# Kernel tuning notes

Hardware: AMD Instinct MI355X
Metric: run time of the kernel (lower is better)

## Reference

```python
import jax, jax.numpy as jnp
import numpy as np

CELL = 50.0  # cubic box edge length (self.cell)
N_ATOMS = 100000
N_PAIRS = 6400000
N_TABLE = 1024
EPS = 1e-12


def setup_inputs() -> dict:
    key = jax.random.key(0)
    k1, k2, k3 = jax.random.split(key, 3)
    # positions inside the box
    q = jax.random.uniform(k1, (N_ATOMS, 3), dtype=jnp.float32) * CELL
    # neighbor pair list [E,2] (each pair listed once; forces scattered to both ends)
    nbr_list = jax.random.randint(k2, (N_PAIRS, 2), 0, N_ATOMS, dtype=jnp.int32)
    # tabulated force: r grid (sorted, covers max minimum-image distance) and force values
    r_max = CELL * np.sqrt(3.0) / 2.0
    table_r = jnp.linspace(0.1, r_max, N_TABLE, dtype=jnp.float32)
    table_f = jax.random.normal(k3, (N_TABLE,), dtype=jnp.float32)
    return {"q": q, "nbr_list": nbr_list, "table_r": table_r, "table_f": table_f}


def reference(q, nbr_list, table_r, table_f):
    i = nbr_list[:, 0]
    j = nbr_list[:, 1]
    # pair displacement with minimum-image convention in a cubic cell
    d = q[i] - q[j]                                  # [E,3]
    d = d - CELL * jnp.round(d / CELL)
    pdist = jnp.sqrt(jnp.sum(d * d, axis=-1, keepdims=True))  # [E,1]
    unit_vector = d / jnp.maximum(pdist, EPS)        # [E,3]
    # tabulated force magnitude lookup (GPU-side interpolation replacing scipy interp1d)
    force_magnitude = jnp.interp(pdist[:, 0], table_r, table_f)[:, None]  # [E,1]
    force_vector = force_magnitude * unit_vector     # [E,3]
    # scatter-add to atoms (index_add_ on dim 0, + on i, - on j)
    force = jnp.zeros_like(q).at[i].add(force_vector).at[j].add(-force_vector)
    return force
```

## Files before the change

### kernel.cpp

```cpp
#include <hip/hip_runtime.h>

#define CELL 50.0f
#define N_TABLE 1024
#define NB 1024
#define NBLK 512
#define THREADS 256
#define SCAT_THREADS 512
#define LBUF_CAP 25088
#define RED_THREADS 512
#define NREP 8
#define BATCH 6

typedef unsigned int uint;
typedef unsigned long long ull;

__global__ __launch_bounds__(THREADS) void pack_q4_kernel(
    const float* __restrict__ q, float4* __restrict__ q4, int n_atoms)
{
    int i = blockIdx.x * THREADS + threadIdx.x;
    if (i < n_atoms)
        q4[i] = make_float4(q[3 * i], q[3 * i + 1], q[3 * i + 2], 0.0f);
}

__global__ __launch_bounds__(THREADS) void hist_kernel(
    const int2* __restrict__ nbr, uint* __restrict__ partial,
    uint* __restrict__ rawh, int n_pairs, int ppb)
{
    __shared__ uint h[NB];
    for (int k = threadIdx.x; k < NB; k += THREADS) h[k] = 0;
    __syncthreads();
    int start = blockIdx.x * ppb;
    int end   = min(start + ppb, n_pairs & ~1);
    const int4* nbr4 = (const int4*)nbr;
    for (int p2 = (start >> 1) + threadIdx.x; p2 < (end >> 1); p2 += THREADS) {
        int4 v = nbr4[p2];
        atomicAdd(&h[((uint)v.x) >> 7], 1u);
        atomicAdd(&h[((uint)v.y) >> 7], 1u);
        atomicAdd(&h[((uint)v.z) >> 7], 1u);
        atomicAdd(&h[((uint)v.w) >> 7], 1u);
    }
    if (blockIdx.x == 0 && threadIdx.x == 0 && (n_pairs & 1)) {
        int2 ij = nbr[n_pairs - 1];
        atomicAdd(&h[((uint)ij.x) >> 7], 1u);
        atomicAdd(&h[((uint)ij.y) >> 7], 1u);
    }
    __syncthreads();
    for (int k = threadIdx.x; k < NB; k += THREADS) {
        uint c = h[k];
        partial[k * NBLK + blockIdx.x] = c;
        rawh[blockIdx.x * NB + k]      = c;
    }
}

__global__ __launch_bounds__(THREADS) void scan_rows_kernel(
    uint* __restrict__ partial, uint* __restrict__ binTotal)
{
    __shared__ uint s[THREADS];
    int bin = blockIdx.x;
    uint running = 0;
    for (int c = 0; c < NBLK / THREADS; c++) {
        int idx = bin * NBLK + c * THREADS + threadIdx.x;
        uint v = partial[idx];
        s[threadIdx.x] = v;
        __syncthreads();
        for (int off = 1; off < THREADS; off <<= 1) {
            uint t = (threadIdx.x >= (uint)off) ? s[threadIdx.x - off] : 0u;
            __syncthreads();
            s[threadIdx.x] += t;
            __syncthreads();
        }
        partial[idx] = running + s[threadIdx.x] - v;
        uint csum = s[THREADS - 1];
        __syncthreads();
        running += csum;
    }
    if (threadIdx.x == 0) binTotal[bin] = running;
}

__global__ __launch_bounds__(THREADS) void scan_totals_kernel(
    const uint* __restrict__ binTotal, uint* __restrict__ binBase)
{
    __shared__ uint s[THREADS];
    uint v[4];
    uint sum = 0;
    int base = threadIdx.x * 4;
    for (int k = 0; k < 4; k++) { v[k] = binTotal[base + k]; sum += v[k]; }
    s[threadIdx.x] = sum;
    __syncthreads();
    for (int off = 1; off < THREADS; off <<= 1) {
        uint t = (threadIdx.x >= (uint)off) ? s[threadIdx.x - off] : 0u;
        __syncthreads();
        s[threadIdx.x] += t;
        __syncthreads();
    }
    uint run = s[threadIdx.x] - sum;
    for (int k = 0; k < 4; k++) { binBase[base + k] = run; run += v[k]; }
    if (threadIdx.x == THREADS - 1) binBase[NB] = run;
}

__global__ __launch_bounds__(SCAT_THREADS) void scatter_sorted_kernel(
    const int2* __restrict__ nbr, const uint* __restrict__ rawh,
    const uint* __restrict__ partial, const uint* __restrict__ binBase,
    uint* __restrict__ entries, int n_pairs, int ppb)
{
    __shared__ uint lbuf[LBUF_CAP];
    __shared__ uint localBase[NB];
    __shared__ uint lcur[NB];
    __shared__ uint gcur[NB];
    __shared__ uint ssc[SCAT_THREADS];

    int tid = threadIdx.x;
    int blk = blockIdx.x;

    for (int k = tid; k < NB; k += SCAT_THREADS)
        gcur[k] = binBase[k] + partial[k * NBLK + blk];

    uint v0 = rawh[blk * NB + 2 * tid];
    uint v1 = rawh[blk * NB + 2 * tid + 1];
    uint sum2 = v0 + v1;
    ssc[tid] = sum2;
    __syncthreads();
    for (int off = 1; off < SCAT_THREADS; off <<= 1) {
        uint t = (tid >= off) ? ssc[tid - off] : 0u;
        __syncthreads();
        ssc[tid] += t;
        __syncthreads();
    }
    uint base = ssc[tid] - sum2;
    localBase[2 * tid]     = base;      lcur[2 * tid]     = base;
    localBase[2 * tid + 1] = base + v0; lcur[2 * tid + 1] = base + v0;
    __syncthreads();

    int start = blk * ppb;
    int end   = min(start + ppb, n_pairs & ~1);
    const int4* nbr4 = (const int4*)nbr;
    int lim = end >> 1;
    int p2  = (start >> 1) + tid;
    if (p2 < lim) {
        int4 v = nbr4[p2];
        for (;;) {
            int pn = p2 + SCAT_THREADS;
            int4 vnext;
            bool has = pn < lim;
            if (has) vnext = nbr4[pn];
            uint i0 = (uint)v.x, j0 = (uint)v.y, i1 = (uint)v.z, j1 = (uint)v.w;
            uint o0 = atomicAdd(&lcur[i0 >> 7], 1u);
            uint o1 = atomicAdd(&lcur[j0 >> 7], 1u);
            uint o2 = atomicAdd(&lcur[i1 >> 7], 1u);
            uint o3 = atomicAdd(&lcur[j1 >> 7], 1u);
            lbuf[o0] = (j0 << 7) | (i0 & 127u);
            lbuf[o1] = (i0 << 7) | (j0 & 127u);
            lbuf[o2] = (j1 << 7) | (i1 & 127u);
            lbuf[o3] = (i1 << 7) | (j1 & 127u);
            if (!has) break;
            v = vnext; p2 = pn;
        }
    }
    if (blk == 0 && tid == 0 && (n_pairs & 1)) {
        int2 ij = nbr[n_pairs - 1];
        uint i = (uint)ij.x, j = (uint)ij.y;
        uint o;
        o = atomicAdd(&lcur[i >> 7], 1u); lbuf[o] = (j << 7) | (i & 127u);
        o = atomicAdd(&lcur[j >> 7], 1u); lbuf[o] = (i << 7) | (j & 127u);
    }
    __syncthreads();

    int wave = tid >> 6, lane = tid & 63;
    for (int b = wave; b < NB; b += SCAT_THREADS / 64) {
        uint lb  = localBase[b];
        uint cnt = lcur[b] - lb;
        if (!cnt) continue;
        uint gdst = gcur[b];
        for (uint o = lane; o < cnt; o += 64)
            entries[gdst + o] = lbuf[lb + o];
    }
}

__global__ __launch_bounds__(THREADS) void scatter_plain_kernel(
    const int2* __restrict__ nbr, const uint* __restrict__ partial,
    const uint* __restrict__ binBase, uint* __restrict__ entries,
    int n_pairs, int ppb)
{
    __shared__ uint cur[NB];
    for (int k = threadIdx.x; k < NB; k += THREADS)
        cur[k] = binBase[k] + partial[k * NBLK + blockIdx.x];
    __syncthreads();
    int start = blockIdx.x * ppb;
    int end   = min(start + ppb, n_pairs & ~1);
    const int4* nbr4 = (const int4*)nbr;
    for (int p2 = (start >> 1) + threadIdx.x; p2 < (end >> 1); p2 += THREADS) {
        int4 v = nbr4[p2];
        uint i0 = (uint)v.x, j0 = (uint)v.y, i1 = (uint)v.z, j1 = (uint)v.w;
        uint p;
        p = atomicAdd(&cur[i0 >> 7], 1u); entries[p] = (j0 << 7) | (i0 & 127u);
        p = atomicAdd(&cur[j0 >> 7], 1u); entries[p] = (i0 << 7) | (j0 & 127u);
        p = atomicAdd(&cur[i1 >> 7], 1u); entries[p] = (j1 << 7) | (i1 & 127u);
        p = atomicAdd(&cur[j1 >> 7], 1u); entries[p] = (i1 << 7) | (j1 & 127u);
    }
    if (blockIdx.x == 0 && threadIdx.x == 0 && (n_pairs & 1)) {
        int2 ij = nbr[n_pairs - 1];
        uint i = (uint)ij.x, j = (uint)ij.y;
        uint p;
        p = atomicAdd(&cur[i >> 7], 1u); entries[p] = (j << 7) | (i & 127u);
        p = atomicAdd(&cur[j >> 7], 1u); entries[p] = (i << 7) | (j & 127u);
    }
}

__device__ __forceinline__ void proc_entry(
    uint ev, float ox, float oy, float oz,
    const float4* __restrict__ qs, const float2* __restrict__ tfp,
    float4* __restrict__ accw, float r0, float inv_dr, int lane)
{
    int local = (int)(ev & 127u);
    float4 m = qs[local];
    float dx = m.x - ox, dy = m.y - oy, dz = m.z - oz;
    dx -= (dx > 25.0f) ? 50.0f : ((dx < -25.0f) ? -50.0f : 0.0f);
    dy -= (dy > 25.0f) ? 50.0f : ((dy < -25.0f) ? -50.0f : 0.0f);
    dz -= (dz > 25.0f) ? 50.0f : ((dz < -25.0f) ? -50.0f : 0.0f);
    float r2 = dx * dx + dy * dy + dz * dz;
    float rs = __builtin_amdgcn_rsqf(fmaxf(r2, 1e-24f));
    float r  = r2 * rs;
    float t  = (r - r0) * inv_dr;
    t = fminf(fmaxf(t, 0.0f), 1023.0f);
    int idx = min((int)t, N_TABLE - 2);
    float frac = t - (float)idx;
    float2 tp = tfp[idx];
    float s = (tp.x + frac * tp.y) * rs;
    float fx = s * dx, fy = s * dy, fz = s * dz;

    ull m64 = __ballot(1);
    #pragma unroll
    for (int b = 0; b < 7; b++) {
        ull bb = __ballot((local >> b) & 1);
        m64 &= ((local >> b) & 1) ? bb : ~bb;
    }
    ull self = 1ull << lane;
    bool leader = ((m64 & (self - 1ull)) == 0ull);
    ull rem = leader ? (m64 & ~self) : 0ull;

    while (__any(rem != 0ull)) {
        int src = rem ? (int)__builtin_ctzll(rem) : lane;
        float px = __shfl(fx, src);
        float py = __shfl(fy, src);
        float pz = __shfl(fz, src);
        if (rem) {
            fx += px; fy += py; fz += pz;
            rem &= rem - 1ull;
        }
    }
    if (leader) {
        float4 a = accw[local];
        a.x += fx; a.y += fy; a.z += fz;
        accw[local] = a;
    }
}

template<int USE_Q4>
__global__ __launch_bounds__(RED_THREADS, 8) void reduce_kernel(
    const float* __restrict__ q, const float4* __restrict__ q4,
    const float* __restrict__ table_r, const float* __restrict__ table_f,
    const uint* __restrict__ binBase, const uint* __restrict__ entries,
    float* __restrict__ force, int n_atoms)
{
    __shared__ float2 tfp[N_TABLE];
    __shared__ float4 qs[128];
    __shared__ float4 accv[NREP * 128];

    int b = blockIdx.x;
    int atomBase = b << 7;
    if (atomBase >= n_atoms) return;
    int nA = min(128, n_atoms - atomBase);
    int lane = threadIdx.x & 63;

    const float r0     = table_r[0];
    const float rend   = table_r[N_TABLE - 1];
    const float inv_dr = (float)(N_TABLE - 1) / (rend - r0);

    for (int k = threadIdx.x; k < N_TABLE - 1; k += RED_THREADS) {
        float a = table_f[k], c = table_f[k + 1];
        tfp[k] = make_float2(a, c - a);
    }
    for (int k = threadIdx.x; k < nA; k += RED_THREADS) {
        if (USE_Q4) qs[k] = q4[atomBase + k];
        else qs[k] = make_float4(q[(atomBase + k) * 3], q[(atomBase + k) * 3 + 1],
                                 q[(atomBase + k) * 3 + 2], 0.0f);
    }
    for (int k = threadIdx.x; k < NREP * 128; k += RED_THREADS)
        accv[k] = make_float4(0.0f, 0.0f, 0.0f, 0.0f);
    __syncthreads();

    float4* accw = &accv[(threadIdx.x >> 6) * 128];

    uint e0 = binBase[b], e1 = binBase[b + 1];
    uint count = e1 - e0;
    const uint CHUNK = BATCH * RED_THREADS;
    uint nmain = (count / CHUNK) * CHUNK;

    if (nmain) {
        uint v[BATCH];
        #pragma unroll
        for (int k = 0; k < BATCH; k++)
            v[k] = entries[e0 + threadIdx.x + k * RED_THREADS];

        for (uint base = 0; base < nmain; ) {
            float ox[BATCH], oy[BATCH], oz[BATCH];
            #pragma unroll
            for (int k = 0; k < BATCH; k++) {
                uint other = v[k] >> 7;
                if (USE_Q4) {
                    const float* p = (const float*)&q4[other];
                    ox[k] = p[0]; oy[k] = p[1]; oz[k] = p[2];
                } else {
                    ox[k] = q[3 * other]; oy[k] = q[3 * other + 1]; oz[k] = q[3 * other + 2];
                }
            }
            uint base_n = base + CHUNK;
            uint vn[BATCH];
            if (base_n < nmain) {
                #pragma unroll
                for (int k = 0; k < BATCH; k++)
                    vn[k] = entries[e0 + base_n + threadIdx.x + k * RED_THREADS];
            } else {
                #pragma unroll
                for (int k = 0; k < BATCH; k++) vn[k] = 0u;
            }
            #pragma unroll
            for (int k = 0; k < BATCH; k++)
                proc_entry(v[k], ox[k], oy[k], oz[k], qs, tfp, accw, r0, inv_dr, lane);
            #pragma unroll
            for (int k = 0; k < BATCH; k++) v[k] = vn[k];
            base = base_n;
        }
    }
    for (uint e = e0 + nmain + threadIdx.x; e < e1; e += RED_THREADS) {
        uint ev = entries[e];
        uint other = ev >> 7;
        float ox, oy, oz;
        if (USE_Q4) {
            const float* p = (const float*)&q4[other];
            ox = p[0]; oy = p[1]; oz = p[2];
        } else {
            ox = q[3 * other]; oy = q[3 * other + 1]; oz = q[3 * other + 2];
        }
        proc_entry(ev, ox, oy, oz, qs, tfp, accw, r0, inv_dr, lane);
    }

    __syncthreads();
    for (int k = threadIdx.x; k < nA; k += RED_THREADS) {
        float sx = 0.0f, sy = 0.0f, sz = 0.0f;
        #pragma unroll
        for (int rp = 0; rp < NREP; rp++) {
            float4 a = accv[rp * 128 + k];
            sx += a.x; sy += a.y; sz += a.z;
        }
        force[(atomBase + k) * 3 + 0] = sx;
        force[(atomBase + k) * 3 + 1] = sy;
        force[(atomBase + k) * 3 + 2] = sz;
    }
}

__global__ __launch_bounds__(THREADS) void pair_force_atomic_kernel(
    const float* __restrict__ q, const int2* __restrict__ nbr,
    const float* __restrict__ table_r, const float* __restrict__ table_f,
    float* __restrict__ force, int n_pairs)
{
    __shared__ float tr[N_TABLE];
    __shared__ float tf[N_TABLE];
    for (int k = threadIdx.x; k < N_TABLE; k += THREADS) { tr[k] = table_r[k]; tf[k] = table_f[k]; }
    __syncthreads();
    const float r0 = tr[0], rend = tr[N_TABLE - 1];
    const float inv_dr = (float)(N_TABLE - 1) / (rend - r0);
    int p = blockIdx.x * THREADS + threadIdx.x;
    if (p >= n_pairs) return;
    int2 ij = nbr[p];
    int i = ij.x, j = ij.y;
    float dx = q[3 * i] - q[3 * j], dy = q[3 * i + 1] - q[3 * j + 1], dz = q[3 * i + 2] - q[3 * j + 2];
    dx -= CELL * rintf(dx / CELL); dy -= CELL * rintf(dy / CELL); dz -= CELL * rintf(dz / CELL);
    float r = sqrtf(dx * dx + dy * dy + dz * dz);
    float inv = 1.0f / fmaxf(r, 1e-12f);
    float fm;
    if (r <= r0) fm = tf[0];
    else if (r >= rend) fm = tf[N_TABLE - 1];
    else {
        float t = (r - r0) * inv_dr;
        int idx = min(max((int)t, 0), N_TABLE - 2);
        if (r < tr[idx]) idx = max(idx - 1, 0);
        else if (r >= tr[idx + 1]) idx = min(idx + 1, N_TABLE - 2);
        float rl = tr[idx], rh = tr[idx + 1];
        fm = tf[idx] + (r - rl) * (tf[idx + 1] - tf[idx]) / (rh - rl);
    }
    float s = fm * inv;
    float fx = s * dx, fy = s * dy, fz = s * dz;
    atomicAdd(&force[3 * i + 0], fx); atomicAdd(&force[3 * i + 1], fy); atomicAdd(&force[3 * i + 2], fz);
    atomicAdd(&force[3 * j + 0], -fx); atomicAdd(&force[3 * j + 1], -fy); atomicAdd(&force[3 * j + 2], -fz);
}

extern "C" void kernel_launch(void* const* d_in, const int* in_sizes, int n_in,
                              void* d_out, int out_size, void* d_ws, size_t ws_size,
                              hipStream_t stream) {
    const float* q       = (const float*)d_in[0];
    const int2*  nbr     = (const int2*)d_in[1];
    const float* table_r = (const float*)d_in[2];
    const float* table_f = (const float*)d_in[3];
    float*       force   = (float*)d_out;

    const int n_pairs = in_sizes[1] / 2;
    const int n_atoms = in_sizes[0] / 3;

    size_t off_partial  = 0;
    size_t off_rawh     = (off_partial + (size_t)NB * NBLK * 4 + 255) & ~255ull;
    size_t off_binTotal = (off_rawh + (size_t)NB * NBLK * 4 + 255) & ~255ull;
    size_t off_binBase  = (off_binTotal + (size_t)NB * 4 + 255) & ~255ull;
    size_t off_entries  = (off_binBase + (size_t)(NB + 1) * 4 + 255) & ~255ull;
    size_t off_q4       = (off_entries + (size_t)2 * n_pairs * 4 + 255) & ~255ull;
    size_t need_base    = off_q4;
    size_t need_q4      = off_q4 + (size_t)n_atoms * 16;

    if (ws_size < need_base || n_atoms > NB * 128) {
        hipMemsetAsync(d_out, 0, (size_t)out_size * sizeof(float), stream);
        int blocks = (n_pairs + THREADS - 1) / THREADS;
        pair_force_atomic_kernel<<<blocks, THREADS, 0, stream>>>(q, nbr, table_r, table_f, force, n_pairs);
        return;
    }

    char* ws = (char*)d_ws;
    uint*   partial  = (uint*)(ws + off_partial);
    uint*   rawh     = (uint*)(ws + off_rawh);
    uint*   binTotal = (uint*)(ws + off_binTotal);
    uint*   binBase  = (uint*)(ws + off_binBase);
    uint*   entries  = (uint*)(ws + off_entries);
    float4* q4       = (float4*)(ws + off_q4);
    int use_q4 = (ws_size >= need_q4) ? 1 : 0;

    int ppb = (((n_pairs + NBLK - 1) / NBLK) + 1) & ~1;

    if (use_q4) {
        int pb = (n_atoms + THREADS - 1) / THREADS;
        pack_q4_kernel<<<pb, THREADS, 0, stream>>>(q, q4, n_atoms);
    }
    hist_kernel<<<NBLK, THREADS, 0, stream>>>(nbr, partial, rawh, n_pairs, ppb);
    scan_rows_kernel<<<NB, THREADS, 0, stream>>>(partial, binTotal);
    scan_totals_kernel<<<1, THREADS, 0, stream>>>(binTotal, binBase);
    if (2 * ppb <= LBUF_CAP)
        scatter_sorted_kernel<<<NBLK, SCAT_THREADS, 0, stream>>>(
            nbr, rawh, partial, binBase, entries, n_pairs, ppb);
    else
        scatter_plain_kernel<<<NBLK, THREADS, 0, stream>>>(
            nbr, partial, binBase, entries, n_pairs, ppb);
    if (use_q4)
        reduce_kernel<1><<<NB, RED_THREADS, 0, stream>>>(q, q4, table_r, table_f, binBase, entries, force, n_atoms);
    else
        reduce_kernel<0><<<NB, RED_THREADS, 0, stream>>>(q, q4, table_r, table_f, binBase, entries, force, n_atoms);
}
```

Before: 171.2 us.

## Sort bin entries by local atom in shared memory and accumulate in registers

The reduce kernel now counting-sorts each bin's entries by local atom index in shared memory, in phases of up to 9216 entries. Four threads then share each atom and accumulate its forces in registers. This replaces the per-entry ballot/shuffle wave-level match-and-reduce and the replicated shared-memory accumulators. The cost is an extra histogram, scan and scatter pass with several block barriers per phase, load imbalance when atoms have uneven neighbour counts, and larger shared memory use that may lower occupancy.

```diff
diff --git a/kernel.cpp b/kernel.cpp
--- a/kernel.cpp
+++ b/kernel.cpp
@@ -8,8 +8,7 @@
 #define SCAT_THREADS 512
 #define LBUF_CAP 25088
 #define RED_THREADS 512
-#define NREP 8
-#define BATCH 6
+#define PHASE_CAP 9216
 
 typedef unsigned int uint;
 typedef unsigned long long ull;
@@ -206,14 +205,12 @@
     }
 }
 
-__device__ __forceinline__ void proc_entry(
-    uint ev, float ox, float oy, float oz,
-    const float4* __restrict__ qs, const float2* __restrict__ tfp,
-    float4* __restrict__ accw, float r0, float inv_dr, int lane)
-{
-    int local = (int)(ev & 127u);
-    float4 m = qs[local];
-    float dx = m.x - ox, dy = m.y - oy, dz = m.z - oz;
+__device__ __forceinline__ void phys_acc(
+    float ax, float ay, float az, float ox, float oy, float oz,
+    const float* __restrict__ tfa, const float* __restrict__ tfd,
+    float r0, float inv_dr, float& fx, float& fy, float& fz)
+{
+    float dx = ax - ox, dy = ay - oy, dz = az - oz;
     dx -= (dx > 25.0f) ? 50.0f : ((dx < -25.0f) ? -50.0f : 0.0f);
     dy -= (dy > 25.0f) ? 50.0f : ((dy < -25.0f) ? -50.0f : 0.0f);
     dz -= (dz > 25.0f) ? 50.0f : ((dz < -25.0f) ? -50.0f : 0.0f);
@@ -224,135 +221,129 @@
     t = fminf(fmaxf(t, 0.0f), 1023.0f);
     int idx = min((int)t, N_TABLE - 2);
     float frac = t - (float)idx;
-    float2 tp = tfp[idx];
-    float s = (tp.x + frac * tp.y) * rs;
-    float fx = s * dx, fy = s * dy, fz = s * dz;
-
-    ull m64 = __ballot(1);
-    #pragma unroll
-    for (int b = 0; b < 7; b++) {
-        ull bb = __ballot((local >> b) & 1);
-        m64 &= ((local >> b) & 1) ? bb : ~bb;
-    }
-    ull self = 1ull << lane;
-    bool leader = ((m64 & (self - 1ull)) == 0ull);
-    ull rem = leader ? (m64 & ~self) : 0ull;
-
-    while (__any(rem != 0ull)) {
-        int src = rem ? (int)__builtin_ctzll(rem) : lane;
-        float px = __shfl(fx, src);
-        float py = __shfl(fy, src);
-        float pz = __shfl(fz, src);
-        if (rem) {
-            fx += px; fy += py; fz += pz;
-            rem &= rem - 1ull;
-        }
-    }
-    if (leader) {
-        float4 a = accw[local];
-        a.x += fx; a.y += fy; a.z += fz;
-        accw[local] = a;
-    }
+    float sm = (tfa[idx] + frac * tfd[idx]) * rs;
+    fx += sm * dx; fy += sm * dy; fz += sm * dz;
 }
 
 template<int USE_Q4>
-__global__ __launch_bounds__(RED_THREADS, 8) void reduce_kernel(
+__global__ __launch_bounds__(RED_THREADS) void reduce_sorted_kernel(
     const float* __restrict__ q, const float4* __restrict__ q4,
     const float* __restrict__ table_r, const float* __restrict__ table_f,
     const uint* __restrict__ binBase, const uint* __restrict__ entries,
     float* __restrict__ force, int n_atoms)
 {
-    __shared__ float2 tfp[N_TABLE];
-    __shared__ float4 qs[128];
-    __shared__ float4 accv[NREP * 128];
-
-    int b = blockIdx.x;
+    __shared__ float tfa[N_TABLE];
+    __shared__ float tfd[N_TABLE];
+    __shared__ uint  sorted[PHASE_CAP];
+    __shared__ uint  hcnt[128], hcur[128], hstart[128], sscan[128];
+    __shared__ float paccx[RED_THREADS], paccy[RED_THREADS], paccz[RED_THREADS];
+
+    int b = blockIdx.x, tid = threadIdx.x;
     int atomBase = b << 7;
     if (atomBase >= n_atoms) return;
     int nA = min(128, n_atoms - atomBase);
-    int lane = threadIdx.x & 63;
 
     const float r0     = table_r[0];
     const float rend   = table_r[N_TABLE - 1];
     const float inv_dr = (float)(N_TABLE - 1) / (rend - r0);
 
-    for (int k = threadIdx.x; k < N_TABLE - 1; k += RED_THREADS) {
-        float a = table_f[k], c = table_f[k + 1];
-        tfp[k] = make_float2(a, c - a);
-    }
-    for (int k = threadIdx.x; k < nA; k += RED_THREADS) {
-        if (USE_Q4) qs[k] = q4[atomBase + k];
-        else qs[k] = make_float4(q[(atomBase + k) * 3], q[(atomBase + k) * 3 + 1],
-                                 q[(atomBase + k) * 3 + 2], 0.0f);
-    }
-    for (int k = threadIdx.x; k < NREP * 128; k += RED_THREADS)
-        accv[k] = make_float4(0.0f, 0.0f, 0.0f, 0.0f);
-    __syncthreads();
-
-    float4* accw = &accv[(threadIdx.x >> 6) * 128];
+    for (int k = tid; k < N_TABLE - 1; k += RED_THREADS) {
+        float a = table_f[k];
+        tfa[k] = a; tfd[k] = table_f[k + 1] - a;
+    }
+    paccx[tid] = 0.0f; paccy[tid] = 0.0f; paccz[tid] = 0.0f;
+
+    int a = tid & 127, s4 = tid >> 7;
+    float ax = 0.0f, ay = 0.0f, az = 0.0f;
+    if (a < nA) {
+        if (USE_Q4) { float4 v = q4[atomBase + a]; ax = v.x; ay = v.y; az = v.z; }
+        else {
+            ax = q[(atomBase + a) * 3];
+            ay = q[(atomBase + a) * 3 + 1];
+            az = q[(atomBase + a) * 3 + 2];
+        }
+    }
 
     uint e0 = binBase[b], e1 = binBase[b + 1];
-    uint count = e1 - e0;
-    const uint CHUNK = BATCH * RED_THREADS;
-    uint nmain = (count / CHUNK) * CHUNK;
-
-    if (nmain) {
-        uint v[BATCH];
-        #pragma unroll
-        for (int k = 0; k < BATCH; k++)
-            v[k] = entries[e0 + threadIdx.x + k * RED_THREADS];
-
-        for (uint base = 0; base < nmain; ) {
-            float ox[BATCH], oy[BATCH], oz[BATCH];
-            #pragma unroll
-            for (int k = 0; k < BATCH; k++) {
-                uint other = v[k] >> 7;
+
+    for (uint es = e0; es < e1; es += PHASE_CAP) {
+        uint ee = min(es + PHASE_CAP, e1);
+
+        if (tid < 128) hcnt[tid] = 0;
+        __syncthreads();
+
+        for (uint e = es + tid; e < ee; e += RED_THREADS)
+            atomicAdd(&hcnt[entries[e] & 127u], 1u);
+        __syncthreads();
+
+        if (tid < 128) sscan[tid] = hcnt[tid];
+        __syncthreads();
+        for (int off = 1; off < 128; off <<= 1) {
+            uint t = 0;
+            if (tid < 128 && tid >= off) t = sscan[tid - off];
+            __syncthreads();
+            if (tid < 128) sscan[tid] += t;
+            __syncthreads();
+        }
+        if (tid < 128) {
+            uint s0 = sscan[tid] - hcnt[tid];
+            hstart[tid] = s0; hcur[tid] = s0;
+        }
+        __syncthreads();
+
+        for (uint e = es + tid; e < ee; e += RED_THREADS) {
+            uint ev = entries[e];
+            uint p  = atomicAdd(&hcur[ev & 127u], 1u);
+            sorted[p] = ev >> 7;
+        }
+        __syncthreads();
+
+        {
+            uint st  = hstart[a];
+            uint cnt = hcnt[a];
+            uint chunk = (cnt + 3) >> 2;
+            uint k0 = min((uint)s4 * chunk, cnt);
+            uint k1 = min(k0 + chunk, cnt);
+            float fx = 0.0f, fy = 0.0f, fz = 0.0f;
+
+            uint k = k0;
+            for (; k + 4 <= k1; k += 4) {
+                uint o0 = sorted[st + k],     o1 = sorted[st + k + 1];
+                uint o2 = sorted[st + k + 2], o3 = sorted[st + k + 3];
+                float x0, y0, z0, x1, y1, z1, x2, y2, z2, x3, y3, z3;
                 if (USE_Q4) {
-                    const float* p = (const float*)&q4[other];
-                    ox[k] = p[0]; oy[k] = p[1]; oz[k] = p[2];
+                    float4 g0 = q4[o0], g1 = q4[o1], g2 = q4[o2], g3 = q4[o3];
+                    x0 = g0.x; y0 = g0.y; z0 = g0.z;
+                    x1 = g1.x; y1 = g1.y; z1 = g1.z;
+                    x2 = g2.x; y2 = g2.y; z2 = g2.z;
+                    x3 = g3.x; y3 = g3.y; z3 = g3.z;
                 } else {
-                    ox[k] = q[3 * other]; oy[k] = q[3 * other + 1]; oz[k] = q[3 * other + 2];
+                    x0 = q[3*o0]; y0 = q[3*o0+1]; z0 = q[3*o0+2];
+                    x1 = q[3*o1]; y1 = q[3*o1+1]; z1 = q[3*o1+2];
+                    x2 = q[3*o2]; y2 = q[3*o2+1]; z2 = q[3*o2+2];
+                    x3 = q[3*o3]; y3 = q[3*o3+1]; z3 = q[3*o3+2];
                 }
+                phys_acc(ax, ay, az, x0, y0, z0, tfa, tfd, r0, inv_dr, fx, fy, fz);
+                phys_acc(ax, ay, az, x1, y1, z1, tfa, tfd, r0, inv_dr, fx, fy, fz);
+                phys_acc(ax, ay, az, x2, y2, z2, tfa, tfd, r0, inv_dr, fx, fy, fz);
+                phys_acc(ax, ay, az, x3, y3, z3, tfa, tfd, r0, inv_dr, fx, fy, fz);
             }
-            uint base_n = base + CHUNK;
-            uint vn[BATCH];
-            if (base_n < nmain) {
-                #pragma unroll
-                for (int k = 0; k < BATCH; k++)
-                    vn[k] = entries[e0 + base_n + threadIdx.x + k * RED_THREADS];
-            } else {
-                #pragma unroll
-                for (int k = 0; k < BATCH; k++) vn[k] = 0u;
+            for (; k < k1; ++k) {
+                uint o = sorted[st + k];
+                float ox, oy, oz;
+                if (USE_Q4) { float4 g = q4[o]; ox = g.x; oy = g.y; oz = g.z; }
+                else { ox = q[3*o]; oy = q[3*o+1]; oz = q[3*o+2]; }
+                phys_acc(ax, ay, az, ox, oy, oz, tfa, tfd, r0, inv_dr, fx, fy, fz);
             }
-            #pragma unroll
-            for (int k = 0; k < BATCH; k++)
-                proc_entry(v[k], ox[k], oy[k], oz[k], qs, tfp, accw, r0, inv_dr, lane);
-            #pragma unroll
-            for (int k = 0; k < BATCH; k++) v[k] = vn[k];
-            base = base_n;
-        }
-    }
-    for (uint e = e0 + nmain + threadIdx.x; e < e1; e += RED_THREADS) {
-        uint ev = entries[e];
-        uint other = ev >> 7;
-        float ox, oy, oz;
-        if (USE_Q4) {
-            const float* p = (const float*)&q4[other];
-            ox = p[0]; oy = p[1]; oz = p[2];
-        } else {
-            ox = q[3 * other]; oy = q[3 * other + 1]; oz = q[3 * other + 2];
-        }
-        proc_entry(ev, ox, oy, oz, qs, tfp, accw, r0, inv_dr, lane);
-    }
-
-    __syncthreads();
-    for (int k = threadIdx.x; k < nA; k += RED_THREADS) {
-        float sx = 0.0f, sy = 0.0f, sz = 0.0f;
-        #pragma unroll
-        for (int rp = 0; rp < NREP; rp++) {
-            float4 a = accv[rp * 128 + k];
-            sx += a.x; sy += a.y; sz += a.z;
-        }
+            paccx[tid] += fx; paccy[tid] += fy; paccz[tid] += fz;
+        }
+        __syncthreads();
+    }
+
+    for (int k = tid; k < nA; k += RED_THREADS) {
+        float sx = paccx[k] + paccx[k + 128] + paccx[k + 256] + paccx[k + 384];
+        float sy = paccy[k] + paccy[k + 128] + paccy[k + 256] + paccy[k + 384];
+        float sz = paccz[k] + paccz[k + 128] + paccz[k + 256] + paccz[k + 384];
         force[(atomBase + k) * 3 + 0] = sx;
         force[(atomBase + k) * 3 + 1] = sy;
         force[(atomBase + k) * 3 + 2] = sz;
@@ -448,7 +439,7 @@
         scatter_plain_kernel<<<NBLK, THREADS, 0, stream>>>(
             nbr, partial, binBase, entries, n_pairs, ppb);
     if (use_q4)
-        reduce_kernel<1><<<NB, RED_THREADS, 0, stream>>>(q, q4, table_r, table_f, binBase, entries, force, n_atoms);
+        reduce_sorted_kernel<1><<<NB, RED_THREADS, 0, stream>>>(q, q4, table_r, table_f, binBase, entries, force, n_atoms);
     else
-        reduce_kernel<0><<<NB, RED_THREADS, 0, stream>>>(q, q4, table_r, table_f, binBase, entries, force, n_atoms);
-}
+        reduce_sorted_kernel<0><<<NB, RED_THREADS, 0, stream>>>(q, q4, table_r, table_f, binBase, entries, force, n_atoms);
+}
```

Measured after the change: 183.6 us. 1.07x slower.
